# Optimization experiments

Measured on AMD Instinct MI355X. Metric: run time of the kernel, lower is better.

## Reference

```python
import jax, jax.numpy as jnp
import numpy as np

B, C, H, W = 8, 64, 64, 64
OUT_CH = 64
K = 3           # kernel_size
STRIDE = 1
PAD = 1
GRID_SIZE = 5
SPLINE_ORDER = 3
GRID_RANGE = (-1.0, 1.0)
IN_FEAT = C * K * K  # 576
N_COEF = GRID_SIZE + SPLINE_ORDER  # 8


def make_grid():
    # (in_feat, grid_size + 2*spline_order + 1) = (576, 12)
    h = (GRID_RANGE[1] - GRID_RANGE[0]) / GRID_SIZE
    g = jnp.arange(-SPLINE_ORDER, GRID_SIZE + SPLINE_ORDER + 1, dtype=jnp.float32) * h + GRID_RANGE[0]
    return jnp.broadcast_to(g, (IN_FEAT, g.shape[0]))


def unfold(x):
    # torch.nn.Unfold: patches ordered (C, kh, kw); output (B, L, C*K*K) rows
    xp = jnp.pad(x, ((0, 0), (0, 0), (PAD, PAD), (PAD, PAD)))
    Hout = (H + 2 * PAD - K) // STRIDE + 1
    Wout = (W + 2 * PAD - K) // STRIDE + 1
    slices = []
    for i in range(K):
        for j in range(K):
            slices.append(xp[:, :, i:i + Hout * STRIDE:STRIDE, j:j + Wout * STRIDE:STRIDE])
    # (B, C, K*K, Hout, Wout) -> (B, C*K*K, L) -> (B*L, C*K*K)
    p = jnp.stack(slices, axis=2)
    p = p.reshape(B, C * K * K, Hout * Wout)
    p = jnp.transpose(p, (0, 2, 1)).reshape(-1, IN_FEAT)
    return p, Hout, Wout


def b_splines(x, grid):
    # x: (N, in), grid: (in, G+2k+1) -> (N, in, G+k)
    xe = x[:, :, None]
    bases = ((xe >= grid[:, :-1]) & (xe < grid[:, 1:])).astype(x.dtype)
    for p in range(1, SPLINE_ORDER + 1):
        left = (xe - grid[:, : -(p + 1)]) / (grid[:, p:-1] - grid[:, : -(p + 1)])
        right = (grid[:, p + 1:] - xe) / (grid[:, p + 1:] - grid[:, 1:-p])
        bases = left * bases[:, :, :-1] + right * bases[:, :, 1:]
    return bases


def setup_inputs() -> dict:
    key = jax.random.key(0)
    k1, k2, k3, k4 = jax.random.split(key, 4)
    return {
        "x": jax.random.normal(k1, (B, C, H, W), dtype=jnp.float32),
        "base_weight": jax.random.normal(k2, (OUT_CH, IN_FEAT), dtype=jnp.float32) * 0.05,
        "spline_weight": jax.random.normal(k3, (OUT_CH, IN_FEAT, N_COEF), dtype=jnp.float32) * 0.05,
        "spline_scaler": jax.random.normal(k4, (OUT_CH, IN_FEAT), dtype=jnp.float32) * 0.05,
    }


def reference(x, base_weight, spline_weight, spline_scaler):
    grid = make_grid()
    patches, Hout, Wout = unfold(x)                    # (B*L, in_feat)
    base_out = jax.nn.silu(patches) @ base_weight.T    # (N, out)
    spl = b_splines(patches, grid)                     # (N, in_feat, G+k)
    scaled_w = spline_weight * spline_scaler[:, :, None]
    spline_out = spl.reshape(spl.shape[0], -1) @ scaled_w.reshape(OUT_CH, -1).T
    out = base_out + spline_out                        # (B*L, out)
    out = out.reshape(B, Hout * Wout, OUT_CH)
    out = jnp.transpose(out, (0, 2, 1)).reshape(B, OUT_CH, Hout, Wout)
    return out
```

## Files before the change

### kernel.cpp

```cpp
#include <hip/hip_runtime.h>
#include <stdint.h>

typedef __bf16 bf16_t;
typedef __bf16 bf16x8 __attribute__((ext_vector_type(8)));
typedef float  f32x4  __attribute__((ext_vector_type(4)));
typedef float  f32x16 __attribute__((ext_vector_type(16)));

#define LDS_TOTAL 49152

__device__ __forceinline__ void gld_lds16(const void* g, void* l) {
  __builtin_amdgcn_global_load_lds(
      (const __attribute__((address_space(1))) uint32_t*)g,
      (__attribute__((address_space(3))) uint32_t*)(uintptr_t)l,
      16, 0, 0);
}

__global__ __launch_bounds__(256) void prep_w_kernel(
    const float* __restrict__ bw, const float* __restrict__ sw,
    const float* __restrict__ ss, bf16_t* __restrict__ Wf2) {
  int idx = blockIdx.x * 256 + threadIdx.x;
  int kk = idx & 15, o = (idx >> 4) & 63, s = idx >> 10;
  int kh = kk >> 3, j = kk & 7;
  float v;
  if (s < 288) {
    int q = s / 9, tap = s - q * 9;
    int c = q * 2 + kh;
    int f = c * 9 + tap;
    v = sw[(o * 576 + f) * 8 + j] * ss[o * 576 + f];
  } else {
    int t2 = s - 288;
    int cq = t2 / 9, tap = t2 - cq * 9;
    int c = cq * 16 + kk;
    int f = c * 9 + tap;
    v = bw[o * 576 + f];
  }
  Wf2[idx] = (bf16_t)v;
}

__global__ __launch_bounds__(256, 2) void convkan_kernel(
    const float* __restrict__ X, const bf16_t* __restrict__ Wf2,
    float* __restrict__ out) {
  extern __shared__ char smraw[];
  char* const Bb0 = smraw;
  char* const Bb1 = smraw + 18432;
  char* const Ab0 = smraw + 36864;
  char* const Ab1 = smraw + 40960;

  const int t    = threadIdx.x;
  const int lane = t & 63;
  const int w    = t >> 6;
  const int r    = lane & 31;
  const int kh   = lane >> 5;

  const int b   = blockIdx.x;
  const int rb  = ((b & 7) << 6) | (b >> 3);
  const int img = rb >> 6;
  const int rem = rb & 63;
  const int ohb = rem >> 3, owb = rem & 7;

  const int h   = t >> 7;
  const int idx = t & 127;
  const int row = idx / 12, col = idx - row * 12;
  const bool valid = (idx < 120) && (col < 10);
  const int ih = ohb * 8 + row - 1;
  const int iw = owb * 8 + col - 1;
  const bool inb = valid && ((unsigned)ih < 64u) && ((unsigned)iw < 64u);
  const float* Ximg = X + (((size_t)img * 64) << 12);
  const int pixoff = (ih << 6) + iw;

  const int khq = kh * 128;
  const int pb0 = (r >> 3) * 12 + (r & 7);
  const int pb1 = pb0 + 48;
  const int tap0 = (w < 3) ? (w * 2) : 6;
  const int ntap = (w < 3) ? 2 : 3;

  const float G0 = -2.2f, G1 = 2.2f, INVH = 2.5f;

  f32x16 acc[2][2];
  #pragma unroll
  for (int a = 0; a < 2; ++a)
    #pragma unroll
    for (int c = 0; c < 2; ++c) acc[a][c] = (f32x16)0.0f;

  auto XLOAD = [&](int cs, float* xr) {
    if (cs < 32) {
      xr[0] = inb ? Ximg[(((size_t)(2 * cs + h)) << 12) + pixoff] : 0.0f;
    } else {
      const int c0 = (cs - 32) * 16 + h * 8;
      #pragma unroll
      for (int j = 0; j < 8; ++j)
        xr[j] = inb ? Ximg[(((size_t)(c0 + j)) << 12) + pixoff] : 0.0f;
    }
  };

  auto WINW = [&](int cs, const float* xr, char* abuf) {
    if (cs < 32) {
      float x  = xr[0];
      float tt = (x - G0) * INVH;
      int  i0  = (int)tt;
      i0 = i0 < 0 ? 0 : (i0 > 10 ? 10 : i0);
      float u  = tt - (float)i0;
      float um = 1.0f - u;
      float u2 = u * u, u3 = u2 * u;
      float w0 = um * um * um * (1.0f / 6.0f);
      float w1 = (3.0f * u3 - 6.0f * u2 + 4.0f) * (1.0f / 6.0f);
      float w2 = (-3.0f * u3 + 3.0f * u2 + 3.0f * u + 1.0f) * (1.0f / 6.0f);
      float w3 = u3 * (1.0f / 6.0f);
      bool inr = (x >= G0) & (x < G1);

      union { bf16_t hh4[4]; unsigned long long u64; } pk;
      pk.hh4[0] = (bf16_t)w0; pk.hh4[1] = (bf16_t)w1;
      pk.hh4[2] = (bf16_t)w2; pk.hh4[3] = (bf16_t)w3;
      unsigned long long a = inr ? pk.u64 : 0ull;

      int sh = (i0 - 3) * 16;
      unsigned long long lo, hi;
      if (sh >= 0) {
        lo = (sh < 64) ? (a << (sh & 63)) : 0ull;
        hi = (sh == 0) ? 0ull
             : ((sh < 64) ? (a >> ((64 - sh) & 63)) : (a << ((sh - 64) & 63)));
      } else {
        lo = a >> ((-sh) & 63);
        hi = 0ull;
      }
      uint4 wv;
      wv.x = (unsigned)(lo & 0xffffffffull); wv.y = (unsigned)(lo >> 32);
      wv.z = (unsigned)(hi & 0xffffffffull); wv.w = (unsigned)(hi >> 32);
      if (valid) *(uint4*)(abuf + ((h * 128 + idx) << 4)) = wv;
    } else {
      union { bf16_t hh8[8]; bf16x8 v; } pk;
      #pragma unroll
      for (int j = 0; j < 8; ++j) {
        float x = xr[j];
        pk.hh8[j] = (bf16_t)(x / (1.0f + __expf(-x)));
      }
      if (valid) *(bf16x8*)(abuf + ((2 * idx + h) << 4)) = pk.v;
    }
  };

  auto STAGEB = [&](int cs, char* bufB) {
    const bf16_t* bsrc = Wf2 + (size_t)(cs < 32 ? cs * 9 : 288 + (cs - 32) * 9) * 1024;
    #pragma unroll
    for (int u = 0; u < 4; ++u)
      gld_lds16(bsrc + ((u * 256 + t) << 3), bufB + ((u * 256 + (w << 6)) << 4));
    if (t < 128)
      gld_lds16(bsrc + ((1024 + t) << 3), bufB + ((1024 + (w << 6)) << 4));
  };

  auto COMPUTE = [&](int ci, const char* bufA, const char* bufB) {
    const bool spline = (ci < 32);
    #pragma unroll
    for (int tt = 0; tt < 3; ++tt) if (tt < ntap) {
      const int tap  = tap0 + tt;
      const int ki   = (tap * 11) >> 5;
      const int koff = ki * 12 + (tap - 3 * ki);
      const int c0 = pb0 + koff, c1 = pb1 + koff;
      const int au0 = spline ? (khq + c0) : (2 * c0 + kh);
      const int au1 = spline ? (khq + c1) : (2 * c1 + kh);
      bf16x8 A0f = *(const bf16x8*)(bufA + (au0 << 4));
      bf16x8 A1f = *(const bf16x8*)(bufA + (au1 << 4));
      const char* bt = bufB + (tap << 11) + r * 32 + kh * 16;
      bf16x8 B0f = *(const bf16x8*)bt;
      bf16x8 B1f = *(const bf16x8*)(bt + 1024);
      acc[0][0] = __builtin_amdgcn_mfma_f32_32x32x16_bf16(A0f, B0f, acc[0][0], 0, 0, 0);
      acc[0][1] = __builtin_amdgcn_mfma_f32_32x32x16_bf16(A0f, B1f, acc[0][1], 0, 0, 0);
      acc[1][0] = __builtin_amdgcn_mfma_f32_32x32x16_bf16(A1f, B0f, acc[1][0], 0, 0, 0);
      acc[1][1] = __builtin_amdgcn_mfma_f32_32x32x16_bf16(A1f, B1f, acc[1][1], 0, 0, 0);
    }
  };

  float xP[8], xQ[8];
  XLOAD(0, xP);
  WINW(0, xP, Ab0);
  XLOAD(1, xP);
  STAGEB(0, Bb0);
  __syncthreads();

  for (int i = 0; i < 18; ++i) {
    {
      const int ci = 2 * i;
      if (ci + 2 < 36) XLOAD(ci + 2, xQ);
      if (ci + 1 < 36) { STAGEB(ci + 1, Bb1); WINW(ci + 1, xP, Ab1); }
      COMPUTE(ci, Ab0, Bb0);
      __syncthreads();
    }
    {
      const int ci = 2 * i + 1;
      if (ci + 2 < 36) XLOAD(ci + 2, xP);
      if (ci + 1 < 36) { STAGEB(ci + 1, Bb0); WINW(ci + 1, xQ, Ab0); }
      COMPUTE(ci, Ab1, Bb1);
      __syncthreads();
    }
  }

  float* red = (float*)smraw;
  if (w != 0) {
    #pragma unroll
    for (int pxt = 0; pxt < 2; ++pxt)
      #pragma unroll
      for (int ot = 0; ot < 2; ++ot)
        #pragma unroll
        for (int q = 0; q < 16; ++q)
          red[(((w - 1) * 64) + (pxt * 2 + ot) * 16 + q) * 64 + lane] = acc[pxt][ot][q];
  }
  __syncthreads();
  if (w == 0) {
    #pragma unroll
    for (int pxt = 0; pxt < 2; ++pxt) {
      #pragma unroll
      for (int ot = 0; ot < 2; ++ot) {
        const int o = ot * 32 + r;
        float* obase = out + (((size_t)(img * 64 + o)) << 12);
        #pragma unroll
        for (int g = 0; g < 4; ++g) {
          f32x4 v;
          #pragma unroll
          for (int iq = 0; iq < 4; ++iq) {
            int q = g * 4 + iq;
            int ri = (pxt * 2 + ot) * 16 + q;
            v[iq] = acc[pxt][ot][q]
                  + red[(0 * 64 + ri) * 64 + lane]
                  + red[(1 * 64 + ri) * 64 + lane]
                  + red[(2 * 64 + ri) * 64 + lane];
          }
          int px = pxt * 32 + 8 * g + 4 * kh;
          *(f32x4*)(obase + (ohb * 8 + (px >> 3)) * 64 + owb * 8 + (px & 7)) = v;
        }
      }
    }
  }
}

extern "C" void kernel_launch(void* const* d_in, const int* in_sizes, int n_in,
                              void* d_out, int out_size, void* d_ws, size_t ws_size,
                              hipStream_t stream) {
  const float* x  = (const float*)d_in[0];
  const float* bw = (const float*)d_in[1];
  const float* sw = (const float*)d_in[2];
  const float* ss = (const float*)d_in[3];

  bf16_t* Wf2 = (bf16_t*)d_ws;
  float*  o   = (float*)d_out;

  prep_w_kernel<<<1296, 256, 0, stream>>>(bw, sw, ss, Wf2);
  convkan_kernel<<<512, 256, LDS_TOTAL, stream>>>(x, Wf2, o);
}
```

Before: 48.96 us.

## Hand-schedule pipeline with fine-grained vmcnt waits and reordered weight layout

Replaces the generic double-buffered loop with an explicitly unrolled pipeline. Each stage issues the weight global-to-LDS copy first, then the x loads, separated by sched_barriers, and closes with a manual s_waitcnt vmcnt(N) plus s_barrier instead of __syncthreads, so the next prefetched x load can stay in flight across the barrier. X loads become branchless (clamped address times mask), and the STAGEB tail load is made unconditional so every thread has the same vmcnt count. The prep kernel reorders weights so kh is the outer index, which makes the B-fragment LDS reads contiguous per lane, and the LDS buffers are resized to match. Hard-coded vmcnt values are fragile if the compiler splits or merges loads, and the extra padding load writes redundant data into LDS.

```diff
diff --git a/kernel.cpp b/kernel.cpp
--- a/kernel.cpp
+++ b/kernel.cpp
@@ -19,8 +19,8 @@
     const float* __restrict__ bw, const float* __restrict__ sw,
     const float* __restrict__ ss, bf16_t* __restrict__ Wf2) {
   int idx = blockIdx.x * 256 + threadIdx.x;
-  int kk = idx & 15, o = (idx >> 4) & 63, s = idx >> 10;
-  int kh = kk >> 3, j = kk & 7;
+  int j = idx & 7, o = (idx >> 3) & 63, kh = (idx >> 9) & 1, s = idx >> 10;
+  int kk = kh * 8 + j;
   float v;
   if (s < 288) {
     int q = s / 9, tap = s - q * 9;
@@ -42,15 +42,13 @@
     float* __restrict__ out) {
   extern __shared__ char smraw[];
   char* const Bb0 = smraw;
-  char* const Bb1 = smraw + 18432;
-  char* const Ab0 = smraw + 36864;
-  char* const Ab1 = smraw + 40960;
+  char* const Bb1 = smraw + 20480;
+  char* const Ab0 = smraw + 40960;
+  char* const Ab1 = smraw + 45056;
 
   const int t    = threadIdx.x;
   const int lane = t & 63;
   const int w    = t >> 6;
-  const int r    = lane & 31;
-  const int kh   = lane >> 5;
 
   const int b   = blockIdx.x;
   const int rb  = ((b & 7) << 6) | (b >> 3);
@@ -66,11 +64,14 @@
   const int iw = owb * 8 + col - 1;
   const bool inb = valid && ((unsigned)ih < 64u) && ((unsigned)iw < 64u);
   const float* Ximg = X + (((size_t)img * 64) << 12);
-  const int pixoff = (ih << 6) + iw;
-
-  const int khq = kh * 128;
-  const int pb0 = (r >> 3) * 12 + (r & 7);
-  const int pb1 = pb0 + 48;
+  const int   psafe = inb ? ((ih << 6) + iw) : 0;
+  const float xmask = inb ? 1.0f : 0.0f;
+
+  const int r    = lane & 31;
+  const int kh   = lane >> 5;
+  const int khq  = kh * 128;
+  const int pb0  = (r >> 3) * 12 + (r & 7);
+  const int pb1  = pb0 + 48;
   const int tap0 = (w < 3) ? (w * 2) : 6;
   const int ntap = (w < 3) ? 2 : 3;
 
@@ -82,14 +83,16 @@
     #pragma unroll
     for (int c = 0; c < 2; ++c) acc[a][c] = (f32x16)0.0f;
 
+  float xP[8], xQ[8];
+
   auto XLOAD = [&](int cs, float* xr) {
     if (cs < 32) {
-      xr[0] = inb ? Ximg[(((size_t)(2 * cs + h)) << 12) + pixoff] : 0.0f;
+      xr[0] = Ximg[(((size_t)(2 * cs + h)) << 12) + psafe] * xmask;
     } else {
       const int c0 = (cs - 32) * 16 + h * 8;
       #pragma unroll
       for (int j = 0; j < 8; ++j)
-        xr[j] = inb ? Ximg[(((size_t)(c0 + j)) << 12) + pixoff] : 0.0f;
+        xr[j] = Ximg[(((size_t)(c0 + j)) << 12) + psafe] * xmask;
     }
   };
 
@@ -143,8 +146,7 @@
     #pragma unroll
     for (int u = 0; u < 4; ++u)
       gld_lds16(bsrc + ((u * 256 + t) << 3), bufB + ((u * 256 + (w << 6)) << 4));
-    if (t < 128)
-      gld_lds16(bsrc + ((1024 + t) << 3), bufB + ((1024 + (w << 6)) << 4));
+    gld_lds16(bsrc + ((t < 128 ? 1024 + t : t) << 3), bufB + ((1024 + (w << 6)) << 4));
   };
 
   auto COMPUTE = [&](int ci, const char* bufA, const char* bufB) {
@@ -159,9 +161,9 @@
       const int au1 = spline ? (khq + c1) : (2 * c1 + kh);
       bf16x8 A0f = *(const bf16x8*)(bufA + (au0 << 4));
       bf16x8 A1f = *(const bf16x8*)(bufA + (au1 << 4));
-      const char* bt = bufB + (tap << 11) + r * 32 + kh * 16;
+      const char* bt = bufB + (tap << 11) + (kh << 10) + (r << 4);
       bf16x8 B0f = *(const bf16x8*)bt;
-      bf16x8 B1f = *(const bf16x8*)(bt + 1024);
+      bf16x8 B1f = *(const bf16x8*)(bt + 512);
       acc[0][0] = __builtin_amdgcn_mfma_f32_32x32x16_bf16(A0f, B0f, acc[0][0], 0, 0, 0);
       acc[0][1] = __builtin_amdgcn_mfma_f32_32x32x16_bf16(A0f, B1f, acc[0][1], 0, 0, 0);
       acc[1][0] = __builtin_amdgcn_mfma_f32_32x32x16_bf16(A1f, B0f, acc[1][0], 0, 0, 0);
@@ -169,30 +171,41 @@
     }
   };
 
-  float xP[8], xQ[8];
+#define BODY(CI, AU, BU, AF, BF, XU, XF, VM, DO_X)                        \
+  do {                                                                     \
+    STAGEB((CI) + 1, BF);                                                  \
+    __builtin_amdgcn_sched_barrier(0);                                     \
+    if (DO_X) XLOAD((CI) + 2, XF);                                         \
+    __builtin_amdgcn_sched_barrier(0);                                     \
+    WINW((CI) + 1, XU, AF);                                                \
+    COMPUTE((CI), AU, BU);                                                 \
+    asm volatile("s_waitcnt vmcnt(" #VM ") lgkmcnt(0)" ::: "memory");      \
+    __builtin_amdgcn_sched_barrier(0);                                     \
+    __builtin_amdgcn_s_barrier();                                          \
+  } while (0)
+
   XLOAD(0, xP);
   WINW(0, xP, Ab0);
+  STAGEB(0, Bb0);
+  __builtin_amdgcn_sched_barrier(0);
   XLOAD(1, xP);
-  STAGEB(0, Bb0);
+  __builtin_amdgcn_sched_barrier(0);
+  asm volatile("s_waitcnt vmcnt(1) lgkmcnt(0)" ::: "memory");
+  __builtin_amdgcn_s_barrier();
+
+  for (int i = 0; i < 15; ++i) {
+    BODY(2 * i,     Ab0, Bb0, Ab1, Bb1, xP, xQ, 1, true);
+    BODY(2 * i + 1, Ab1, Bb1, Ab0, Bb0, xQ, xP, 1, true);
+  }
+  BODY(30, Ab0, Bb0, Ab1, Bb1, xP, xQ, 8, true);
+  BODY(31, Ab1, Bb1, Ab0, Bb0, xQ, xP, 8, true);
+  BODY(32, Ab0, Bb0, Ab1, Bb1, xP, xQ, 8, true);
+  BODY(33, Ab1, Bb1, Ab0, Bb0, xQ, xP, 8, true);
+  BODY(34, Ab0, Bb0, Ab1, Bb1, xP, xQ, 0, false);
+  COMPUTE(35, Ab1, Bb1);
+#undef BODY
+
   __syncthreads();
-
-  for (int i = 0; i < 18; ++i) {
-    {
-      const int ci = 2 * i;
-      if (ci + 2 < 36) XLOAD(ci + 2, xQ);
-      if (ci + 1 < 36) { STAGEB(ci + 1, Bb1); WINW(ci + 1, xP, Ab1); }
-      COMPUTE(ci, Ab0, Bb0);
-      __syncthreads();
-    }
-    {
-      const int ci = 2 * i + 1;
-      if (ci + 2 < 36) XLOAD(ci + 2, xP);
-      if (ci + 1 < 36) { STAGEB(ci + 1, Bb0); WINW(ci + 1, xQ, Ab0); }
-      COMPUTE(ci, Ab1, Bb1);
-      __syncthreads();
-    }
-  }
-
   float* red = (float*)smraw;
   if (w != 0) {
     #pragma unroll
```

Result: no change. 48.93 us (-0.1%).

## Load weight fragments directly into registers instead of staging through LDS

Applied to the files above, without the earlier changes.

Weight fragments are no longer staged in LDS with global_load_lds. Each wave now loads the B operands it needs straight from global memory into registers, double-buffered across iterations, and the prep kernel's weight layout is changed so each lane's fragment is contiguous. This frees 36KB of LDS and removes the LDS read traffic for B. The cost is more VGPRs, and each wave issues its own global loads, served from L2, with no sharing through LDS. Input loads also become branchless by using a clamped address times a mask.

```diff
diff --git a/kernel.cpp b/kernel.cpp
--- a/kernel.cpp
+++ b/kernel.cpp
@@ -8,19 +8,12 @@
 
 #define LDS_TOTAL 49152
 
-__device__ __forceinline__ void gld_lds16(const void* g, void* l) {
-  __builtin_amdgcn_global_load_lds(
-      (const __attribute__((address_space(1))) uint32_t*)g,
-      (__attribute__((address_space(3))) uint32_t*)(uintptr_t)l,
-      16, 0, 0);
-}
-
 __global__ __launch_bounds__(256) void prep_w_kernel(
     const float* __restrict__ bw, const float* __restrict__ sw,
     const float* __restrict__ ss, bf16_t* __restrict__ Wf2) {
   int idx = blockIdx.x * 256 + threadIdx.x;
-  int kk = idx & 15, o = (idx >> 4) & 63, s = idx >> 10;
-  int kh = kk >> 3, j = kk & 7;
+  int j = idx & 7, o = (idx >> 3) & 63, kh = (idx >> 9) & 1, s = idx >> 10;
+  int kk = kh * 8 + j;
   float v;
   if (s < 288) {
     int q = s / 9, tap = s - q * 9;
@@ -41,16 +34,12 @@
     const float* __restrict__ X, const bf16_t* __restrict__ Wf2,
     float* __restrict__ out) {
   extern __shared__ char smraw[];
-  char* const Bb0 = smraw;
-  char* const Bb1 = smraw + 18432;
-  char* const Ab0 = smraw + 36864;
-  char* const Ab1 = smraw + 40960;
+  char* const Ab0 = smraw;
+  char* const Ab1 = smraw + 4096;
 
   const int t    = threadIdx.x;
   const int lane = t & 63;
   const int w    = t >> 6;
-  const int r    = lane & 31;
-  const int kh   = lane >> 5;
 
   const int b   = blockIdx.x;
   const int rb  = ((b & 7) << 6) | (b >> 3);
@@ -66,11 +55,14 @@
   const int iw = owb * 8 + col - 1;
   const bool inb = valid && ((unsigned)ih < 64u) && ((unsigned)iw < 64u);
   const float* Ximg = X + (((size_t)img * 64) << 12);
-  const int pixoff = (ih << 6) + iw;
-
-  const int khq = kh * 128;
-  const int pb0 = (r >> 3) * 12 + (r & 7);
-  const int pb1 = pb0 + 48;
+  const int   psafe = inb ? ((ih << 6) + iw) : 0;
+  const float xmask = inb ? 1.0f : 0.0f;
+
+  const int r    = lane & 31;
+  const int kh   = lane >> 5;
+  const int khq  = kh * 128;
+  const int pb0  = (r >> 3) * 12 + (r & 7);
+  const int pb1  = pb0 + 48;
   const int tap0 = (w < 3) ? (w * 2) : 6;
   const int ntap = (w < 3) ? 2 : 3;
 
@@ -82,14 +74,27 @@
     #pragma unroll
     for (int c = 0; c < 2; ++c) acc[a][c] = (f32x16)0.0f;
 
+  float xP[8], xQ[8];
+  bf16x8 BP[3][2], BQ[3][2];
+
   auto XLOAD = [&](int cs, float* xr) {
     if (cs < 32) {
-      xr[0] = inb ? Ximg[(((size_t)(2 * cs + h)) << 12) + pixoff] : 0.0f;
+      xr[0] = Ximg[(((size_t)(2 * cs + h)) << 12) + psafe] * xmask;
     } else {
       const int c0 = (cs - 32) * 16 + h * 8;
       #pragma unroll
       for (int j = 0; j < 8; ++j)
-        xr[j] = inb ? Ximg[(((size_t)(c0 + j)) << 12) + pixoff] : 0.0f;
+        xr[j] = Ximg[(((size_t)(c0 + j)) << 12) + psafe] * xmask;
+    }
+  };
+
+  auto BLOAD = [&](int cs, bf16x8 (*BB)[2]) {
+    const int sb = (cs < 32) ? cs * 9 : 288 + (cs - 32) * 9;
+    #pragma unroll
+    for (int tt = 0; tt < 3; ++tt) if (tt < ntap) {
+      const bf16_t* p = Wf2 + (((size_t)(sb + tap0 + tt)) << 10) + (kh << 9) + (r << 3);
+      BB[tt][0] = *(const bf16x8*)p;
+      BB[tt][1] = *(const bf16x8*)(p + 256);
     }
   };
 
@@ -138,16 +143,7 @@
     }
   };
 
-  auto STAGEB = [&](int cs, char* bufB) {
-    const bf16_t* bsrc = Wf2 + (size_t)(cs < 32 ? cs * 9 : 288 + (cs - 32) * 9) * 1024;
-    #pragma unroll
-    for (int u = 0; u < 4; ++u)
-      gld_lds16(bsrc + ((u * 256 + t) << 3), bufB + ((u * 256 + (w << 6)) << 4));
-    if (t < 128)
-      gld_lds16(bsrc + ((1024 + t) << 3), bufB + ((1024 + (w << 6)) << 4));
-  };
-
-  auto COMPUTE = [&](int ci, const char* bufA, const char* bufB) {
+  auto COMPUTE = [&](int ci, const char* bufA, bf16x8 (*BB)[2]) {
     const bool spline = (ci < 32);
     #pragma unroll
     for (int tt = 0; tt < 3; ++tt) if (tt < ntap) {
@@ -159,36 +155,32 @@
       const int au1 = spline ? (khq + c1) : (2 * c1 + kh);
       bf16x8 A0f = *(const bf16x8*)(bufA + (au0 << 4));
       bf16x8 A1f = *(const bf16x8*)(bufA + (au1 << 4));
-      const char* bt = bufB + (tap << 11) + r * 32 + kh * 16;
-      bf16x8 B0f = *(const bf16x8*)bt;
-      bf16x8 B1f = *(const bf16x8*)(bt + 1024);
-      acc[0][0] = __builtin_amdgcn_mfma_f32_32x32x16_bf16(A0f, B0f, acc[0][0], 0, 0, 0);
-      acc[0][1] = __builtin_amdgcn_mfma_f32_32x32x16_bf16(A0f, B1f, acc[0][1], 0, 0, 0);
-      acc[1][0] = __builtin_amdgcn_mfma_f32_32x32x16_bf16(A1f, B0f, acc[1][0], 0, 0, 0);
-      acc[1][1] = __builtin_amdgcn_mfma_f32_32x32x16_bf16(A1f, B1f, acc[1][1], 0, 0, 0);
-    }
-  };
-
-  float xP[8], xQ[8];
+      acc[0][0] = __builtin_amdgcn_mfma_f32_32x32x16_bf16(A0f, BB[tt][0], acc[0][0], 0, 0, 0);
+      acc[0][1] = __builtin_amdgcn_mfma_f32_32x32x16_bf16(A0f, BB[tt][1], acc[0][1], 0, 0, 0);
+      acc[1][0] = __builtin_amdgcn_mfma_f32_32x32x16_bf16(A1f, BB[tt][0], acc[1][0], 0, 0, 0);
+      acc[1][1] = __builtin_amdgcn_mfma_f32_32x32x16_bf16(A1f, BB[tt][1], acc[1][1], 0, 0, 0);
+    }
+  };
+
   XLOAD(0, xP);
   WINW(0, xP, Ab0);
+  BLOAD(0, BP);
   XLOAD(1, xP);
-  STAGEB(0, Bb0);
   __syncthreads();
 
   for (int i = 0; i < 18; ++i) {
     {
       const int ci = 2 * i;
       if (ci + 2 < 36) XLOAD(ci + 2, xQ);
-      if (ci + 1 < 36) { STAGEB(ci + 1, Bb1); WINW(ci + 1, xP, Ab1); }
-      COMPUTE(ci, Ab0, Bb0);
+      if (ci + 1 < 36) { BLOAD(ci + 1, BQ); WINW(ci + 1, xP, Ab1); }
+      COMPUTE(ci, Ab0, BP);
       __syncthreads();
     }
     {
       const int ci = 2 * i + 1;
       if (ci + 2 < 36) XLOAD(ci + 2, xP);
-      if (ci + 1 < 36) { STAGEB(ci + 1, Bb0); WINW(ci + 1, xQ, Ab0); }
-      COMPUTE(ci, Ab1, Bb1);
+      if (ci + 1 < 36) { BLOAD(ci + 1, BP); WINW(ci + 1, xQ, Ab0); }
+      COMPUTE(ci, Ab1, BQ);
       __syncthreads();
     }
   }
```

Measured after the change: 54.15 us. +10.6%, slower.
